# Optimization experiments

Measured on AMD Instinct MI355X. Metric: run time of the kernel, lower is better.

Reference implementation:

```python
import math
import jax, jax.numpy as jnp
import numpy as np
from jax.scipy.special import xlogy, gammaln

HEADS = 8
DIM_KEY = 64
NUM_REL_POS_FEATURES = 192


def get_positional_embed(n, feature_size):
    # distances: [-n+1, ..., n-1], length 2n-1
    dist = jnp.arange(-n + 1, n)
    adist = jnp.abs(dist).astype(jnp.float32)[:, None]  # (2n-1, 1)
    num_basis = feature_size // 6  # 3 feature fns * 2 (sign-augmented)
    seq_len = n
    # exponential half-life features
    max_range = math.log(seq_len) / math.log(2.0)
    half_life = 2.0 ** jnp.linspace(3.0, max_range, num_basis)  # min_half_life=3.0
    feat_exp = jnp.exp(-math.log(2.0) / half_life[None, :] * adist)
    # central mask features
    center_widths = 2.0 ** jnp.arange(1, num_basis + 1) - 1.0
    feat_cm = (center_widths[None, :] > adist).astype(jnp.float32)
    # gamma pdf features
    stddev = seq_len / (2 * num_basis)
    start_mean = seq_len / num_basis
    mean = jnp.linspace(start_mean, float(seq_len), num_basis)[None, :]
    concentration = (mean / stddev) ** 2
    rate = mean / (stddev ** 2)
    log_unnorm = xlogy(concentration - 1.0, adist) - rate * adist
    log_norm = gammaln(concentration) - concentration * jnp.log(rate)
    prob = jnp.exp(log_unnorm - log_norm) + 1e-8
    feat_gamma = prob / jnp.max(prob, axis=-1, keepdims=True)
    emb = jnp.concatenate([feat_exp, feat_cm, feat_gamma], axis=-1)  # (2n-1, fs/2)
    sign = jnp.sign(dist).astype(jnp.float32)[:, None]
    return jnp.concatenate([emb, sign * emb], axis=-1)  # (2n-1, fs)


def relative_shift(x):
    # x: (b, h, n, 2n-1) -> (b, h, n, n) Transformer-XL shift
    b, h, t1, t2 = x.shape
    x = jnp.pad(x, ((0, 0), (0, 0), (0, 0), (1, 0)))  # (b,h,t1,t2+1)
    x = x.reshape(b, h, t2 + 1, t1)[:, :, 1:, :].reshape(b, h, t1, t2)
    return x[..., : (t2 + 2) // 2]


def setup_inputs() -> dict:
    key = jax.random.key(0)
    ks = jax.random.split(key, 8)
    dim = 1536
    b, n = 2, 1536
    hdk = HEADS * DIM_KEY  # 512
    hdv = HEADS * 192      # 1536
    s = 0.02
    return {
        'x': jax.random.normal(ks[0], (b, n, dim), jnp.float32),
        'Wq': jax.random.normal(ks[1], (hdk, dim), jnp.float32) * s,
        'Wk': jax.random.normal(ks[2], (hdk, dim), jnp.float32) * s,
        'Wv': jax.random.normal(ks[3], (hdv, dim), jnp.float32) * s,
        'Wrel': jax.random.normal(ks[4], (hdk, NUM_REL_POS_FEATURES), jnp.float32) * s,
        'Wout': jax.random.normal(ks[5], (dim, hdv), jnp.float32) * s,
        'b_out': jnp.zeros((dim,), jnp.float32),
        'rel_content_bias': jax.random.normal(ks[6], (1, HEADS, 1, DIM_KEY), jnp.float32),
        'rel_pos_bias': jax.random.normal(ks[7], (1, HEADS, 1, DIM_KEY), jnp.float32),
    }


def reference(x, Wq, Wk, Wv, Wrel, Wout, b_out, rel_content_bias, rel_pos_bias):
    b, n, dim = x.shape
    h = HEADS
    scale = DIM_KEY ** -0.5

    def split_heads(t):  # (b, n, h*d) -> (b, h, n, d)
        return t.reshape(b, n, h, -1).transpose(0, 2, 1, 3)

    q = split_heads(jnp.einsum('bnd,fd->bnf', x, Wq)) * scale
    k = split_heads(jnp.einsum('bnd,fd->bnf', x, Wk))
    v = split_heads(jnp.einsum('bnd,fd->bnf', x, Wv))

    content_logits = jnp.einsum('bhid,bhjd->bhij', q + rel_content_bias, k)

    positions = get_positional_embed(n, NUM_REL_POS_FEATURES)  # (2n-1, fs)
    rel_k = jnp.einsum('jf,ef->je', positions, Wrel).reshape(2 * n - 1, h, DIM_KEY)
    rel_k = rel_k.transpose(1, 0, 2)  # (h, 2n-1, dk)
    rel_logits = jnp.einsum('bhid,hjd->bhij', q + rel_pos_bias, rel_k)
    rel_logits = relative_shift(rel_logits)  # (b, h, n, n)

    attn = jax.nn.softmax(content_logits + rel_logits, axis=-1)
    out = jnp.einsum('bhij,bhjd->bhid', attn, v)
    out = out.transpose(0, 2, 1, 3).reshape(b, n, -1)  # (b, n, h*dv)
    return jnp.einsum('bnf,df->bnd', out, Wout) + b_out
```

## Files before the change

kernel.cpp:

```cpp
#include <hip/hip_runtime.h>
#include <cmath>

typedef unsigned short u16;
typedef unsigned int u32;
typedef short frag8 __attribute__((ext_vector_type(8)));
typedef float f32x4 __attribute__((ext_vector_type(4)));

#define DEVINL __device__ __forceinline__

DEVINL float bf2f(u16 v) { return __uint_as_float(((u32)v) << 16); }
DEVINL u16 f2bf(float f) {
    u32 u = __float_as_uint(f);
    u32 r = (u + 0x7fffu + ((u >> 16) & 1u)) >> 16;
    return (u16)r;
}
DEVINL u32 pack2(float a, float b) { return (u32)f2bf(a) | ((u32)f2bf(b) << 16); }
DEVINL void async_copy16(const u16* g, u16* l) {
    __builtin_amdgcn_global_load_lds((const __attribute__((address_space(1))) u32*)g,
                                     (__attribute__((address_space(3))) u32*)l, 16, 0, 0);
}
DEVINL f32x4 mfma_bf16(frag8 a, frag8 b, f32x4 c) {
    return __builtin_amdgcn_mfma_f32_16x16x32_bf16(a, b, c, 0, 0, 0);
}
#define VMCNT(N) asm volatile("s_waitcnt vmcnt(" #N ")" ::: "memory")
DEVINL void bar_raw() {
    asm volatile("s_waitcnt lgkmcnt(0)" ::: "memory");
    __builtin_amdgcn_s_barrier();
    asm volatile("" ::: "memory");
}

__global__ __launch_bounds__(256) void convert_kernel(
        const float* __restrict__ s0, const float* __restrict__ s1,
        const float* __restrict__ s2, const float* __restrict__ s3,
        const float* __restrict__ s4, u16* __restrict__ dst) {
    const int c0 = 589824, c1 = 98304, c2 = 98304, c3 = 294912;
    const int total = 1376256;
    for (int c = blockIdx.x * blockDim.x + threadIdx.x; c < total;
         c += gridDim.x * blockDim.x) {
        const float* src; int off;
        if (c < c0) { src = s0; off = c; }
        else if (c < c0 + c1) { src = s1; off = c - c0; }
        else if (c < c0 + c1 + c2) { src = s2; off = c - c0 - c1; }
        else if (c < c0 + c1 + c2 + c3) { src = s3; off = c - c0 - c1 - c2; }
        else { src = s4; off = c - c0 - c1 - c2 - c3; }
        float4 a = ((const float4*)src)[off * 2];
        float4 b = ((const float4*)src)[off * 2 + 1];
        uint4 o;
        o.x = pack2(a.x, a.y); o.y = pack2(a.z, a.w);
        o.z = pack2(b.x, b.y); o.w = pack2(b.z, b.w);
        ((uint4*)dst)[c] = o;
    }
}

DEVINL double lgamma_stirling(double z) {
    double zi = 1.0 / z, zi2 = zi * zi;
    return (z - 0.5) * log(z) - z + 0.91893853320467274178
         + zi * (1.0 / 12.0) - zi * zi2 * (1.0 / 360.0) + zi * zi2 * zi2 * (1.0 / 1260.0);
}

__global__ __launch_bounds__(256) void embed_relk_kernel(const float* __restrict__ Wrel,
                                                         u16* __restrict__ relk) {
    __shared__ float pos[16][192];
    __shared__ float inv_hl[32], cwid[32], cm1[32], rateS[32];
    __shared__ double lognS[32];
    __shared__ float gmax[16];
    int t = threadIdx.x;
    int u0b = blockIdx.x * 16;

    if (t < 32) {
        double step = (10.584962500721156 - 3.0) / 31.0;
        double hl = exp2(3.0 + t * step);
        inv_hl[t] = (float)(1.0 / hl);
        cwid[t] = exp2f((float)(t + 1)) - 1.0f;
        double mean = 48.0 * (t + 1);
        double conc = (mean / 24.0) * (mean / 24.0);
        double rate = mean / 576.0;
        cm1[t] = (float)(conc - 1.0);
        rateS[t] = (float)rate;
        lognS[t] = lgamma_stirling(conc) - conc * log(rate);
    }
    __syncthreads();

    for (int idx = t; idx < 512; idx += 256) {
        int ul = idx >> 5, bs = idx & 31;
        int dist = u0b + ul - 1535;
        float ad = fabsf((float)dist);
        pos[ul][bs] = exp2f(-ad * inv_hl[bs]);
        pos[ul][32 + bs] = (cwid[bs] > ad) ? 1.0f : 0.0f;
        double prob = 0.0;
        if (dist != 0) {
            double adD = (double)ad;
            prob = exp((double)cm1[bs] * log(adD) - (double)rateS[bs] * adD - lognS[bs]);
        }
        pos[ul][64 + bs] = (float)(prob + 1e-8);
    }
    __syncthreads();
    if (t < 16) {
        float g = 0.f;
        #pragma unroll
        for (int bsx = 0; bsx < 32; bsx++) g = fmaxf(g, pos[t][64 + bsx]);
        gmax[t] = g;
    }
    __syncthreads();
    for (int idx = t; idx < 16 * 96; idx += 256) {
        int ul = idx / 96, f = idx - ul * 96;
        float v = pos[ul][f];
        if (f >= 64) { v = v / gmax[ul]; pos[ul][f] = v; }
        int dist = u0b + ul - 1535;
        float sg = (dist > 0) ? 1.f : ((dist < 0) ? -1.f : 0.f);
        pos[ul][96 + f] = sg * v;
    }
    __syncthreads();

    int e0 = t * 2;
    const float* w0 = Wrel + e0 * 192;
    const float* w1 = w0 + 192;
    float a0[16], a1[16];
    #pragma unroll
    for (int ul = 0; ul < 16; ul++) { a0[ul] = 0.f; a1[ul] = 0.f; }
    for (int f = 0; f < 192; f++) {
        float wa = w0[f], wb = w1[f];
        #pragma unroll
        for (int ul = 0; ul < 16; ul++) {
            float p = pos[ul][f];
            a0[ul] = fmaf(p, wa, a0[ul]);
            a1[ul] = fmaf(p, wb, a1[ul]);
        }
    }
    int h0 = e0 >> 6, d0 = e0 & 63;
    int h1 = (e0 + 1) >> 6, d1 = (e0 + 1) & 63;
    for (int ul = 0; ul < 16; ul++) {
        int u = u0b + ul;
        relk[(h0 * 3072 + u) * 64 + d0] = f2bf(a0[ul]);
        relk[(h1 * 3072 + u) * 64 + d1] = f2bf(a1[ul]);
    }
}

DEVINL void gemm128_stage(const u16* __restrict__ A, const u16* __restrict__ B,
                          int K, int k0, u16* buf, int tid) {
    #pragma unroll
    for (int p = 0; p < 2; p++) {
        int e = (p * 256 + tid) * 8;
        int r = e >> 5, c = e & 31;
        async_copy16(A + r * K + k0 + c, buf + e);
        async_copy16(B + r * K + k0 + c, buf + 4096 + e);
    }
}

DEVINL void gemm128_mainloop(const u16* __restrict__ A, const u16* __restrict__ B,
                             int K, f32x4 acc[4][4], u16* smem) {
    int tid = threadIdx.x;
    int lane = tid & 63, wave = tid >> 6;
    int wm = (wave >> 1) * 64, wn = (wave & 1) * 64;
    int fm = lane & 15, fq = lane >> 4;
    const int NT = K >> 5;
    gemm128_stage(A, B, K, 0,  smem,         tid);
    gemm128_stage(A, B, K, 32, smem + 8192,  tid);
    gemm128_stage(A, B, K, 64, smem + 16384, tid);
    for (int t = 0; t < NT; t++) {
        u16* cur = smem + (t & 3) * 8192;
        if (t + 3 < NT) {
            gemm128_stage(A, B, K, (t + 3) * 32, smem + ((t + 3) & 3) * 8192, tid);
            VMCNT(12);
        } else if (t + 2 < NT) {
            VMCNT(8);
        } else if (t + 1 < NT) {
            VMCNT(4);
        } else {
            VMCNT(0);
        }
        bar_raw();
        frag8 af[4], bfr[4];
        #pragma unroll
        for (int mi = 0; mi < 4; mi++) af[mi] = *(const frag8*)&cur[(wm + 16 * mi + fm) * 32 + fq * 8];
        #pragma unroll
        for (int ni = 0; ni < 4; ni++) bfr[ni] = *(const frag8*)&cur[4096 + (wn + 16 * ni + fm) * 32 + fq * 8];
        #pragma unroll
        for (int mi = 0; mi < 4; mi++)
            #pragma unroll
            for (int ni = 0; ni < 4; ni++)
                acc[mi][ni] = mfma_bf16(af[mi], bfr[ni], acc[mi][ni]);
        bar_raw();
    }
}

__global__ __launch_bounds__(256) void gemm_qkv_kernel(
        const u16* __restrict__ X, const u16* __restrict__ Wq, const u16* __restrict__ Wk,
        const u16* __restrict__ Wv, const float* __restrict__ cbias, const float* __restrict__ pbias,
        u16* __restrict__ qc, u16* __restrict__ qp, u16* __restrict__ kws, u16* __restrict__ vt) {
    __shared__ __align__(16) u16 smem[32768];
    int flat = blockIdx.y * 24 + blockIdx.x;
    int nf   = (flat & 7) * 60 + (flat >> 3);
    int m0 = (nf % 24) * 128, n0 = (nf / 24) * 128;
    const u16* Bp; int brow;
    if (n0 < 512)       { Bp = Wq; brow = n0; }
    else if (n0 < 1024) { Bp = Wk; brow = n0 - 512; }
    else                { Bp = Wv; brow = n0 - 1024; }
    f32x4 acc[4][4];
    #pragma unroll
    for (int i = 0; i < 4; i++)
        #pragma unroll
        for (int j = 0; j < 4; j++) acc[i][j] = (f32x4){0.f, 0.f, 0.f, 0.f};
    gemm128_mainloop(X + m0 * 1536, Bp + brow * 1536, 1536, acc, smem);

    int tid = threadIdx.x, lane = tid & 63, wave = tid >> 6;
    int wm = (wave >> 1) * 64, wn = (wave & 1) * 64, fm = lane & 15, fq = lane >> 4;
    #pragma unroll
    for (int mi = 0; mi < 4; mi++) {
        #pragma unroll
        for (int ni = 0; ni < 4; ni++) {
            int col = n0 + wn + 16 * ni + fm;
            int rbase = m0 + wm + 16 * mi + fq * 4;
            #pragma unroll
            for (int reg = 0; reg < 4; reg++) {
                int row = rbase + reg;
                float v = acc[mi][ni][reg];
                int b = row >= 1536 ? 1 : 0;
                int i = row - b * 1536;
                if (n0 < 512) {
                    float qv = v * 0.125f;
                    int idx = ((b * 8 + (col >> 6)) * 1536 + i) * 64 + (col & 63);
                    qc[idx] = f2bf(qv + cbias[col]);
                    qp[idx] = f2bf(qv + pbias[col]);
                } else if (n0 < 1024) {
                    int c2 = col - 512;
                    kws[((b * 8 + (c2 >> 6)) * 1536 + i) * 64 + (c2 & 63)] = f2bf(v);
                } else {
                    int c2 = col - 1024;
                    int hh = c2 / 192, dd = c2 - hh * 192;
                    vt[((b * 8 + hh) * 192 + dd) * 1536 + i] = f2bf(v);
                }
            }
        }
    }
}

DEVINL void stage_k(const u16* kP, u16* k_lds, int j0, int tid) {
    #pragma unroll
    for (int p = 0; p < 2; p++) {
        int l = p * 256 + tid, r = l >> 3, c = (l & 7) ^ (r & 7);
        async_copy16(kP + (j0 + r) * 64 + c * 8, k_lds + l * 8);
    }
}
DEVINL void stage_relk(const u16* rkP, u16* relk_lds, int u0, int tid) {
    #pragma unroll
    for (int p = 0; p < 3; p++) {
        int l = p * 256 + tid, r = l >> 3, c = (l & 7) ^ (r & 7);
        async_copy16(rkP + (u0 + r) * 64 + c * 8, relk_lds + l * 8);
    }
}
DEVINL void stage_v(const u16* vtP, u16* vt_lds, int j0, int tid) {
    #pragma unroll
    for (int p = 0; p < 6; p++) {
        int l = p * 256 + tid, r = l >> 3, c = (l & 7) ^ (r & 7);
        async_copy16(vtP + r * 1536 + j0 + c * 8, vt_lds + l * 8);
    }
}

__global__ __launch_bounds__(256) void attn_kernel(
        const u16* __restrict__ qc, const u16* __restrict__ qp, const u16* __restrict__ kws,
        const u16* __restrict__ vt, const u16* __restrict__ relk, u16* __restrict__ ao) {
    __shared__ __align__(16) u16 smem[24768];
    u16* k_lds    = smem;
    u16* vt_lds   = smem + 4096;
    u16* relk_lds = smem + 16384;
    u16* P_lds    = smem + 22528;
    float* S_lds  = (float*)k_lds;
    float* R_lds  = (float*)relk_lds;
    float* mstate = (float*)(smem + 24576);
    float* lstate = mstate + 32;
    float* alpha_lds = lstate + 32;

    const int n = 1536;
    int flat = blockIdx.y * 48 + blockIdx.x;
    int swz  = (flat & 7) * 96 + (flat >> 3);
    int bh = swz / 48;
    int i0 = (swz - bh * 48) * 32;
    int b = bh >> 3, h = bh & 7;
    const u16* qcP = qc + bh * n * 64;
    const u16* qpP = qp + bh * n * 64;
    const u16* kP  = kws + bh * n * 64;
    const u16* vtP = vt + bh * 192 * n;
    const u16* rkP = relk + h * 3072 * 64;

    int tid = threadIdx.x, lane = tid & 63, w = tid >> 6, fm = lane & 15, fq = lane >> 4;
    int sw = fm & 7;
    if (tid < 32) { mstate[tid] = __int_as_float(0xff800000); lstate[tid] = 0.f; }

    frag8 aqc[2][2], aqp[2][2];
    #pragma unroll
    for (int mi = 0; mi < 2; mi++)
        #pragma unroll
        for (int ks = 0; ks < 2; ks++) {
            int off = (i0 + 16 * mi + fm) * 64 + ks * 32 + fq * 8;
            aqc[mi][ks] = *(const frag8*)(qcP + off);
            aqp[mi][ks] = *(const frag8*)(qpP + off);
        }

    f32x4 acc_o[2][3];
    #pragma unroll
    for (int mi = 0; mi < 2; mi++)
        #pragma unroll
        for (int dj = 0; dj < 3; dj++) acc_o[mi][dj] = (f32x4){0.f, 0.f, 0.f, 0.f};

    int uis[3], rmis[3];
    #pragma unroll
    for (int tt = 0; tt < 3; tt++) {
        int tv = w + tt * 4;
        rmis[tt] = (tv >= 6) ? 1 : 0;
        uis[tt] = tv - rmis[tt] * 6;
    }

    stage_k(kP, k_lds, 0, tid);
    stage_relk(rkP, relk_lds, 1504 - i0, tid);

    for (int jt = 0; jt < 24; jt++) {
        int j0 = jt * 64;
        bar_raw();
        stage_v(vtP, vt_lds, j0, tid);
        VMCNT(6);
        bar_raw();

        f32x4 acc_s[2];
        acc_s[0] = (f32x4){0.f, 0.f, 0.f, 0.f};
        acc_s[1] = (f32x4){0.f, 0.f, 0.f, 0.f};
        #pragma unroll
        for (int ks = 0; ks < 2; ks++) {
            frag8 bk = *(const frag8*)&k_lds[(16 * w + fm) * 64 + ((ks * 4 + fq) ^ sw) * 8];
            acc_s[0] = mfma_bf16(aqc[0][ks], bk, acc_s[0]);
            acc_s[1] = mfma_bf16(aqc[1][ks], bk, acc_s[1]);
        }
        f32x4 acc_r[3];
        #pragma unroll
        for (int tt = 0; tt < 3; tt++) {
            acc_r[tt] = (f32x4){0.f, 0.f, 0.f, 0.f};
            #pragma unroll
            for (int ks = 0; ks < 2; ks++) {
                frag8 br = *(const frag8*)&relk_lds[(16 * uis[tt] + fm) * 64 + ((ks * 4 + fq) ^ sw) * 8];
                acc_r[tt] = mfma_bf16(aqp[rmis[tt]][ks], br, acc_r[tt]);
            }
        }
        bar_raw();

        #pragma unroll
        for (int mi = 0; mi < 2; mi++)
            #pragma unroll
            for (int reg = 0; reg < 4; reg++)
                S_lds[(16 * mi + fq * 4 + reg) * 64 + 16 * w + fm] = acc_s[mi][reg];
        #pragma unroll
        for (int tt = 0; tt < 3; tt++)
            #pragma unroll
            for (int reg = 0; reg < 4; reg++)
                R_lds[(16 * rmis[tt] + fq * 4 + reg) * 96 + 16 * uis[tt] + fm] = acc_r[tt][reg];
        bar_raw();

        int li = tid >> 3, c0 = (tid & 7) * 8;
        float sv[8];
        float mx = __int_as_float(0xff800000);
        #pragma unroll
        for (int e = 0; e < 8; e++) {
            int c = c0 + e;
            sv[e] = S_lds[li * 64 + c] + R_lds[li * 96 + c - li + 31];
            mx = fmaxf(mx, sv[e]);
        }
        mx = fmaxf(mx, __shfl_xor(mx, 1));
        mx = fmaxf(mx, __shfl_xor(mx, 2));
        mx = fmaxf(mx, __shfl_xor(mx, 4));
        float mo = mstate[li];
        float mn = fmaxf(mo, mx);
        float al = __expf(mo - mn);
        float pe[8], sum = 0.f;
        #pragma unroll
        for (int e = 0; e < 8; e++) { pe[e] = __expf(sv[e] - mn); sum += pe[e]; }
        {
            uint4 pw;
            pw.x = pack2(pe[0], pe[1]); pw.y = pack2(pe[2], pe[3]);
            pw.z = pack2(pe[4], pe[5]); pw.w = pack2(pe[6], pe[7]);
            int slot = (tid & 7) ^ (li & 7);
            *(uint4*)&P_lds[li * 64 + slot * 8] = pw;
        }
        sum += __shfl_xor(sum, 1);
        sum += __shfl_xor(sum, 2);
        sum += __shfl_xor(sum, 4);
        if ((tid & 7) == 0) {
            mstate[li] = mn;
            lstate[li] = lstate[li] * al + sum;
            alpha_lds[li] = al;
        }
        VMCNT(0);
        bar_raw();

        if (jt < 23) {
            stage_k(kP, k_lds, j0 + 64, tid);
            stage_relk(rkP, relk_lds, 1504 - i0 + j0 + 64, tid);
        }

        #pragma unroll
        for (int mi = 0; mi < 2; mi++)
            #pragma unroll
            for (int reg = 0; reg < 4; reg++) {
                float al2 = alpha_lds[16 * mi + fq * 4 + reg];
                #pragma unroll
                for (int dj = 0; dj < 3; dj++) acc_o[mi][dj][reg] *= al2;
            }
        frag8 ap[2][2];
        #pragma unroll
        for (int mi = 0; mi < 2; mi++)
            #pragma unroll
            for (int ks = 0; ks < 2; ks++)
                ap[mi][ks] = *(const frag8*)&P_lds[(16 * mi + fm) * 64 + ((ks * 4 + fq) ^ sw) * 8];
        #pragma unroll
        for (int dj = 0; dj < 3; dj++) {
            #pragma unroll
            for (int ks = 0; ks < 2; ks++) {
                frag8 bv = *(const frag8*)&vt_lds[(16 * (3 * w + dj) + fm) * 64 + ((ks * 4 + fq) ^ sw) * 8];
                acc_o[0][dj] = mfma_bf16(ap[0][ks], bv, acc_o[0][dj]);
                acc_o[1][dj] = mfma_bf16(ap[1][ks], bv, acc_o[1][dj]);
            }
        }
    }

    #pragma unroll
    for (int mi = 0; mi < 2; mi++)
        #pragma unroll
        for (int dj = 0; dj < 3; dj++)
            #pragma unroll
            for (int reg = 0; reg < 4; reg++) {
                int rl = 16 * mi + fq * 4 + reg;
                float lsum = lstate[rl];
                int row = b * 1536 + i0 + rl;
                int col = h * 192 + 16 * (3 * w + dj) + fm;
                ao[row * 1536 + col] = f2bf(acc_o[mi][dj][reg] / lsum);
            }
}

__global__ __launch_bounds__(256) void gemm_out_kernel(
        const u16* __restrict__ A, const u16* __restrict__ W, const float* __restrict__ bias,
        float* __restrict__ out) {
    __shared__ __align__(16) u16 smem[32768];
    int flat = blockIdx.y * 24 + blockIdx.x;
    int nf   = (flat & 7) * 36 + (flat >> 3);
    int m0 = (nf % 24) * 128, n0 = (nf / 24) * 128;
    f32x4 acc[4][4];
    #pragma unroll
    for (int i = 0; i < 4; i++)
        #pragma unroll
        for (int j = 0; j < 4; j++) acc[i][j] = (f32x4){0.f, 0.f, 0.f, 0.f};
    gemm128_mainloop(A + m0 * 1536, W + n0 * 1536, 1536, acc, smem);

    int tid = threadIdx.x, lane = tid & 63, wave = tid >> 6;
    int wm = (wave >> 1) * 64, wn = (wave & 1) * 64, fm = lane & 15, fq = lane >> 4;
    #pragma unroll
    for (int mi = 0; mi < 4; mi++) {
        #pragma unroll
        for (int ni = 0; ni < 4; ni++) {
            int col = n0 + wn + 16 * ni + fm;
            int rbase = m0 + wm + 16 * mi + fq * 4;
            float bv = bias[col];
            #pragma unroll
            for (int reg = 0; reg < 4; reg++) {
                int row = rbase + reg;
                out[row * 1536 + col] = acc[mi][ni][reg] + bv;
            }
        }
    }
}

extern "C" void kernel_launch(void* const* d_in, const int* in_sizes, int n_in,
                              void* d_out, int out_size, void* d_ws, size_t ws_size,
                              hipStream_t stream) {
    (void)in_sizes; (void)n_in; (void)out_size; (void)ws_size;
    const float* x    = (const float*)d_in[0];
    const float* Wq   = (const float*)d_in[1];
    const float* Wk   = (const float*)d_in[2];
    const float* Wv   = (const float*)d_in[3];
    const float* Wrel = (const float*)d_in[4];
    const float* Wout = (const float*)d_in[5];
    const float* bout = (const float*)d_in[6];
    const float* cb   = (const float*)d_in[7];
    const float* pb   = (const float*)d_in[8];

    u16* xb  = (u16*)d_ws;
    u16* wqb = xb  + 4718592;
    u16* wkb = wqb + 786432;
    u16* wvb = wkb + 786432;
    u16* wob = wvb + 2359296;
    u16* qc  = wob + 2359296;
    u16* qp  = qc + 1572864;
    u16* kw  = qp + 1572864;
    u16* vt  = kw + 1572864;
    u16* rk  = vt + 4718592;
    u16* ao  = rk + 1572864;
    float* out = (float*)d_out;

    convert_kernel<<<dim3(1024), dim3(256), 0, stream>>>(x, Wq, Wk, Wv, Wout, xb);
    embed_relk_kernel<<<dim3(192), dim3(256), 0, stream>>>(Wrel, rk);
    gemm_qkv_kernel<<<dim3(24, 20), dim3(256), 0, stream>>>(xb, wqb, wkb, wvb, cb, pb, qc, qp, kw, vt);
    attn_kernel<<<dim3(48, 16), dim3(256), 0, stream>>>(qc, qp, kw, vt, rk, ao);
    gemm_out_kernel<<<dim3(24, 12), dim3(256), 0, stream>>>(ao, wob, bout, out);
}
```

Measured before the change: 300.0 us.

## Load V fragments directly to registers and give S/R dedicated padded LDS

Drops V staging through LDS: each wave loads its V^T MFMA B-fragments straight from global memory into registers at the start of each tile, so those loads overlap the QK and rel-pos MFMAs. S and R score buffers move to their own LDS regions with padded strides, which lets the next K/rel-K async prefetch be issued right after the score MFMAs instead of after softmax. Softmax reads S with vectorized float4 loads. This shrinks LDS use and shortens the serialized per-tile chain, at the cost of more VGPRs and uncoalesced-per-wave global V reads that bypass LDS sharing.

```diff
diff --git a/kernel.cpp b/kernel.cpp
--- a/kernel.cpp
+++ b/kernel.cpp
@@ -249,25 +249,20 @@
         async_copy16(rkP + (u0 + r) * 64 + c * 8, relk_lds + l * 8);
     }
 }
-DEVINL void stage_v(const u16* vtP, u16* vt_lds, int j0, int tid) {
-    #pragma unroll
-    for (int p = 0; p < 6; p++) {
-        int l = p * 256 + tid, r = l >> 3, c = (l & 7) ^ (r & 7);
-        async_copy16(vtP + r * 1536 + j0 + c * 8, vt_lds + l * 8);
-    }
-}
+
+#define SP 68
+#define RP 100
 
 __global__ __launch_bounds__(256) void attn_kernel(
         const u16* __restrict__ qc, const u16* __restrict__ qp, const u16* __restrict__ kws,
         const u16* __restrict__ vt, const u16* __restrict__ relk, u16* __restrict__ ao) {
-    __shared__ __align__(16) u16 smem[24768];
+    __shared__ __align__(16) u16 smem[23232];
     u16* k_lds    = smem;
-    u16* vt_lds   = smem + 4096;
-    u16* relk_lds = smem + 16384;
-    u16* P_lds    = smem + 22528;
-    float* S_lds  = (float*)k_lds;
-    float* R_lds  = (float*)relk_lds;
-    float* mstate = (float*)(smem + 24576);
+    u16* relk_lds = smem + 4096;
+    u16* P_lds    = smem + 10240;
+    float* S_lds  = (float*)(smem + 12288);
+    float* R_lds  = (float*)(smem + 16640);
+    float* mstate = (float*)(smem + 23040);
     float* lstate = mstate + 32;
     float* alpha_lds = lstate + 32;
 
@@ -316,10 +311,16 @@
 
     for (int jt = 0; jt < 24; jt++) {
         int j0 = jt * 64;
+        VMCNT(0);
         bar_raw();
-        stage_v(vtP, vt_lds, j0, tid);
-        VMCNT(6);
-        bar_raw();
+
+        frag8 fv[3][2];
+        #pragma unroll
+        for (int dj = 0; dj < 3; dj++)
+            #pragma unroll
+            for (int ks = 0; ks < 2; ks++)
+                fv[dj][ks] = *(const frag8*)(vtP + (48 * w + 16 * dj + fm) * 1536
+                                             + j0 + (4 * ks + fq) * 8);
 
         f32x4 acc_s[2];
         acc_s[0] = (f32x4){0.f, 0.f, 0.f, 0.f};
@@ -342,25 +343,36 @@
         }
         bar_raw();
 
+        if (jt < 23) {
+            stage_k(kP, k_lds, j0 + 64, tid);
+            stage_relk(rkP, relk_lds, 1504 - i0 + j0 + 64, tid);
+        }
+
         #pragma unroll
         for (int mi = 0; mi < 2; mi++)
             #pragma unroll
             for (int reg = 0; reg < 4; reg++)
-                S_lds[(16 * mi + fq * 4 + reg) * 64 + 16 * w + fm] = acc_s[mi][reg];
+                S_lds[(16 * mi + fq * 4 + reg) * SP + 16 * w + fm] = acc_s[mi][reg];
         #pragma unroll
         for (int tt = 0; tt < 3; tt++)
             #pragma unroll
             for (int reg = 0; reg < 4; reg++)
-                R_lds[(16 * rmis[tt] + fq * 4 + reg) * 96 + 16 * uis[tt] + fm] = acc_r[tt][reg];
+                R_lds[(16 * rmis[tt] + fq * 4 + reg) * RP + 16 * uis[tt] + fm] = acc_r[tt][reg];
         bar_raw();
 
         int li = tid >> 3, c0 = (tid & 7) * 8;
         float sv[8];
+        {
+            float4 sa = *(const float4*)(S_lds + li * SP + c0);
+            float4 sb = *(const float4*)(S_lds + li * SP + c0 + 4);
+            sv[0] = sa.x; sv[1] = sa.y; sv[2] = sa.z; sv[3] = sa.w;
+            sv[4] = sb.x; sv[5] = sb.y; sv[6] = sb.z; sv[7] = sb.w;
+        }
+        const float* rrow = R_lds + li * RP + c0 - li + 31;
         float mx = __int_as_float(0xff800000);
         #pragma unroll
         for (int e = 0; e < 8; e++) {
-            int c = c0 + e;
-            sv[e] = S_lds[li * 64 + c] + R_lds[li * 96 + c - li + 31];
+            sv[e] += rrow[e];
             mx = fmaxf(mx, sv[e]);
         }
         mx = fmaxf(mx, __shfl_xor(mx, 1));
@@ -387,13 +399,7 @@
             lstate[li] = lstate[li] * al + sum;
             alpha_lds[li] = al;
         }
-        VMCNT(0);
         bar_raw();
-
-        if (jt < 23) {
-            stage_k(kP, k_lds, j0 + 64, tid);
-            stage_relk(rkP, relk_lds, 1504 - i0 + j0 + 64, tid);
-        }
 
         #pragma unroll
         for (int mi = 0; mi < 2; mi++)
@@ -413,9 +419,8 @@
         for (int dj = 0; dj < 3; dj++) {
             #pragma unroll
             for (int ks = 0; ks < 2; ks++) {
-                frag8 bv = *(const frag8*)&vt_lds[(16 * (3 * w + dj) + fm) * 64 + ((ks * 4 + fq) ^ sw) * 8];
-                acc_o[0][dj] = mfma_bf16(ap[0][ks], bv, acc_o[0][dj]);
-                acc_o[1][dj] = mfma_bf16(ap[1][ks], bv, acc_o[1][dj]);
+                acc_o[0][dj] = mfma_bf16(ap[0][ks], fv[dj][ks], acc_o[0][dj]);
+                acc_o[1][dj] = mfma_bf16(ap[1][ks], fv[dj][ks], acc_o[1][dj]);
             }
         }
     }
```

Result: slower. 317.9 us (+6.0%).
